# Optimization experiments

Measured on AMD Instinct MI355X. Metric: run time of the kernel, lower is better.

Reference implementation:

```python
import jax, jax.numpy as jnp
import numpy as np

PENALTY = -100.0  # reset penalty used by the torch module


def log_g(x):
    # torch: where(x >= 0, log(relu(x) + 0.5), -softplus(-x))
    return jnp.where(x >= 0, jnp.log(jax.nn.relu(x) + 0.5), -jax.nn.softplus(-x))


def setup_inputs() -> dict:
    key = jax.random.key(0)
    k1, k2, k3 = jax.random.split(key, 3)
    B, S, D = 4, 8192, 1024
    x = jax.random.normal(k1, (B, S, D), dtype=jnp.float32)
    W = jax.random.normal(k2, (D, 2 * D), dtype=jnp.float32) * (1.0 / np.sqrt(D))
    input_ids = jax.random.randint(k3, (B, S), 0, 32000, dtype=jnp.int64)
    return {"x": x, "W": W, "input_ids": input_ids}


def reference(x, W, input_ids):
    # x: [B,S,D], W: [D,2D] (to_hidden_and_gate, no bias), proj_out=False -> Identity
    hg = jnp.einsum("bsd,de->bse", x, W)            # [B,S,2D]
    hidden, gate = jnp.split(hg, 2, axis=-1)          # each [B,S,D]

    pad_mask = input_ids == 0                         # [B,S]

    log_coeffs = -jax.nn.softplus(gate)               # log(1 - z)
    log_z = -jax.nn.softplus(-gate)                   # log z
    log_values = log_z + log_g(hidden)                # log(z * h_tilde)

    # reset at positions following a pad token (shifted mask)
    reset = jnp.pad(pad_mask[:, :-1], ((0, 0), (1, 0)))[:, :, None]  # [B,S,1]

    lc = jnp.where(reset, PENALTY, log_coeffs)
    a_star = jnp.cumsum(lc, axis=1)
    lv = jnp.where(reset, PENALTY, log_values)
    log_h = a_star + jax.lax.cumlogsumexp(lv - a_star, axis=1)
    out = jnp.exp(log_h)                              # [B,S,D]

    next_prev_hidden = jnp.where(pad_mask[:, -1:, None], 0.0, out[:, -1:])
    return out, next_prev_hidden
```

## Files before the change

kernel.cpp:

```cpp
#include <hip/hip_runtime.h>
#include <hip/hip_fp16.h>
#include <math.h>

#define S_LEN 8192
#define D_DIM 1024
#define B_DIM 4
#define M_DIM (B_DIM * S_LEN)
#define BSD   ((size_t)M_DIM * D_DIM)
#define CHN   (B_DIM * D_DIM)
#define CHUNK 64
#define NCH   (S_LEN / CHUNK)

typedef _Float16 f16x8 __attribute__((ext_vector_type(8)));
typedef __attribute__((ext_vector_type(4))) float f32x4;
typedef unsigned int u32;

__device__ __forceinline__ u32 pk2h(float a, float b) {
    auto h = __builtin_amdgcn_cvt_pkrtz(a, b);
    u32 r; __builtin_memcpy(&r, &h, 4); return r;
}

__device__ __forceinline__ void gload16(const void* g, void* l) {
    __builtin_amdgcn_global_load_lds(
        (const __attribute__((address_space(1))) u32*)g,
        (__attribute__((address_space(3))) u32*)l,
        16, 0, 0);
}

__global__ __launch_bounds__(256) void w_to_f16t(
    const float* __restrict__ W, unsigned short* __restrict__ Wt)
{
    __shared__ float T[64][65];
    const int t  = threadIdx.x;
    const int n0 = (int)blockIdx.x * 64;
    const int k0 = (int)blockIdx.y * 64;
    #pragma unroll
    for (int p = 0; p < 4; ++p) {
        int u = p * 256 + t;
        int r = u >> 4, c4 = (u & 15) * 4;
        float4 v = *(const float4*)&W[(size_t)(k0 + r) * 2048 + n0 + c4];
        T[r][c4 + 0] = v.x; T[r][c4 + 1] = v.y;
        T[r][c4 + 2] = v.z; T[r][c4 + 3] = v.w;
    }
    __syncthreads();
    #pragma unroll
    for (int p = 0; p < 2; ++p) {
        int u = p * 256 + t;
        int n = u >> 3, kc = (u & 7) * 8;
        u32 out[4];
        #pragma unroll
        for (int j = 0; j < 4; ++j)
            out[j] = pk2h(T[kc + 2 * j][n], T[kc + 2 * j + 1][n]);
        *(uint4*)&Wt[(size_t)(n0 + n) * 1024 + k0 + kc] = *(uint4*)out;
    }
}

__global__ __launch_bounds__(256) void x_to_f16sw(
    const float* __restrict__ x, unsigned short* __restrict__ xh)
{
    int tid = (int)blockIdx.x * 256 + threadIdx.x;
    int m  = tid >> 7;
    int cg = tid & 127;
    const float4* src = (const float4*)&x[(size_t)m * 1024 + cg * 8];
    float4 v0 = src[0], v1 = src[1];
    u32 o[4] = { pk2h(v0.x, v0.y), pk2h(v0.z, v0.w),
                 pk2h(v1.x, v1.y), pk2h(v1.z, v1.w) };
    int j   = cg & 7;
    int cgd = (cg & ~7) | (j ^ (m & 7));
    *(uint4*)&xh[(size_t)m * 1024 + cgd * 8] = *(uint4*)o;
}

__global__ __launch_bounds__(512, 2) void gemm_8p(
    const unsigned short* __restrict__ xh, const unsigned short* __restrict__ Wt,
    const int* __restrict__ ids, u32* __restrict__ P)
{
    __shared__ __align__(16) unsigned short Ah[2 * 256 * 64];
    __shared__ __align__(16) unsigned short Bt[2 * 256 * 64];

    const int t    = threadIdx.x;
    const int lane = t & 63;
    const int wid  = t >> 6;
    const int wm   = wid >> 2;
    const int wd   = wid & 3;

    const int lin  = (int)blockIdx.x;
    const int xcd  = lin & 7;
    const int slot = lin >> 3;
    const int m0   = (xcd * 16 + (slot >> 3)) * 256;
    const int c0   = (slot & 7) * 128;

    f32x4 accH[8][2], accG[8][2];
    #pragma unroll
    for (int i = 0; i < 8; ++i)
        #pragma unroll
        for (int j = 0; j < 2; ++j) {
            accH[i][j] = (f32x4)0.0f;
            accG[i][j] = (f32x4)0.0f;
        }

    auto stageA = [&](int kb, int buf, int half) {
        char* Ad = (char*)Ah + (buf << 15) + (half << 14);
        #pragma unroll
        for (int i = 0; i < 2; ++i) {
            int sl  = i * 512 + t;
            int row = half * 128 + (sl >> 3);
            int c   = sl & 7;
            const unsigned short* src =
                xh + ((size_t)(m0 + row) << 10) + kb + (c << 3);
            gload16(src, Ad + (size_t)sl * 16);
        }
    };
    auto stageB = [&](int kb, int buf, int half) {
        char* Bd = (char*)Bt + (buf << 15) + (half << 14);
        #pragma unroll
        for (int i = 0; i < 2; ++i) {
            int sl  = i * 512 + t;
            int col = sl >> 3;
            int kc  = (sl & 7) ^ (col & 7);
            const unsigned short* src =
                Wt + ((size_t)(half * 1024 + c0 + col) << 10) + kb + (kc << 3);
            gload16(src, Bd + (size_t)sl * 16);
        }
    };

    auto readA = [&](const char* Ab, int kk, f16x8 a[8]) {
        int chunk = kk * 4 + (lane >> 4);
        #pragma unroll
        for (int mf = 0; mf < 8; ++mf) {
            int row = wm * 128 + mf * 16 + (lane & 15);
            a[mf] = *(const f16x8*)(Ab + row * 128 + ((chunk ^ (row & 7)) << 4));
        }
    };
    auto readB = [&](const char* Bb, int kk, int hg, f16x8 b[2]) {
        int chunk = kk * 4 + (lane >> 4);
        #pragma unroll
        for (int df = 0; df < 2; ++df) {
            int col = wd * 32 + df * 16 + (lane & 15);
            b[df] = *(const f16x8*)(Bb + (hg * 128 + col) * 128
                                       + ((chunk ^ (col & 7)) << 4));
        }
    };

    #define MMA_CLUSTER(ACC, AV, BV)                                       \
        __builtin_amdgcn_s_setprio(1);                                     \
        _Pragma("unroll")                                                  \
        for (int mf = 0; mf < 8; ++mf)                                     \
            _Pragma("unroll")                                              \
            for (int df = 0; df < 2; ++df)                                 \
                ACC[mf][df] = __builtin_amdgcn_mfma_f32_16x16x32_f16(      \
                    AV[mf], BV[df], ACC[mf][df], 0, 0, 0);                 \
        __builtin_amdgcn_s_setprio(0);

    stageA(0, 0, 0); stageA(0, 0, 1); stageB(0, 0, 0); stageB(0, 0, 1);
    asm volatile("s_waitcnt vmcnt(0)" ::: "memory");
    __builtin_amdgcn_sched_barrier(0);
    __builtin_amdgcn_s_barrier();

    for (int tt = 0; tt < 16; ++tt) {
        const int buf   = tt & 1;
        const int kbn   = (tt + 1) << 6;
        const bool more = tt < 15;
        const char* Ab = (const char*)Ah + (buf << 15);
        const char* Bb = (const char*)Bt + (buf << 15);
        f16x8 a0[8], a1[8], bh0[2], bg0[2], bh1[2], bg1[2];

        readA(Ab, 0, a0); readB(Bb, 0, 0, bh0);
        if (more) { stageA(kbn, buf ^ 1, 0); stageA(kbn, buf ^ 1, 1); }
        asm volatile("s_waitcnt lgkmcnt(0)" ::: "memory");
        __builtin_amdgcn_sched_barrier(0);
        readB(Bb, 0, 1, bg0);
        __builtin_amdgcn_sched_barrier(0);
        MMA_CLUSTER(accH, a0, bh0)

        asm volatile("s_waitcnt lgkmcnt(0)" ::: "memory");
        __builtin_amdgcn_sched_barrier(0);
        readA(Ab, 1, a1); readB(Bb, 1, 0, bh1);
        if (more) { stageB(kbn, buf ^ 1, 0); stageB(kbn, buf ^ 1, 1); }
        __builtin_amdgcn_sched_barrier(0);
        MMA_CLUSTER(accG, a0, bg0)

        asm volatile("s_waitcnt lgkmcnt(0)" ::: "memory");
        __builtin_amdgcn_sched_barrier(0);
        readB(Bb, 1, 1, bg1);
        __builtin_amdgcn_sched_barrier(0);
        MMA_CLUSTER(accH, a1, bh1)

        asm volatile("s_waitcnt lgkmcnt(0)" ::: "memory");
        __builtin_amdgcn_sched_barrier(0);
        MMA_CLUSTER(accG, a1, bg1)
        if (more) {
            asm volatile("s_waitcnt vmcnt(0)" ::: "memory");
            __builtin_amdgcn_sched_barrier(0);
            __builtin_amdgcn_s_barrier();
        }
    }
    #undef MMA_CLUSTER

    #pragma unroll
    for (int mf = 0; mf < 8; ++mf) {
        int mbase = m0 + wm * 128 + mf * 16 + (lane >> 4) * 4;
        #pragma unroll
        for (int r = 0; r < 4; ++r) {
            int m = mbase + r;
            int b = m >> 13;
            int s = m & 8191;
            bool reset = (s > 0) && (ids[b * S_LEN + s - 1] == 0);
            #pragma unroll
            for (int df = 0; df < 2; ++df) {
                int d = c0 + wd * 32 + df * 16 + (lane & 15);
                float hid = accH[mf][df][r];
                float g   = accG[mf][df][r];
                float eg  = __expf(-g);
                float z   = 1.0f / (1.0f + eg);
                float c   = eg * z;
                float gt  = (hid >= 0.0f) ? (hid + 0.5f)
                                          : 1.0f / (1.0f + __expf(-hid));
                float v   = z * gt;
                if (reset) { c = 0.0f; v = 0.0f; }
                __half2 h2 = __floats2half2_rn(c, v);
                u32 packed;
                __builtin_memcpy(&packed, &h2, 4);
                P[(size_t)m * D_DIM + d] = packed;
            }
        }
    }
}

__global__ __launch_bounds__(256, 3) void gemm_fb(
    const float* __restrict__ x, const unsigned short* __restrict__ Wt,
    const int* __restrict__ ids, u32* __restrict__ P)
{
    __shared__ __align__(16) unsigned short Ah[128 * 64];
    __shared__ __align__(16) unsigned short Bt[2 * 64 * 64];

    const int t    = threadIdx.x;
    const int lane = t & 63;
    const int wid  = t >> 6;
    const int wm   = wid >> 1;
    const int wd   = wid & 1;

    const int lin  = (int)blockIdx.y * (int)gridDim.x + (int)blockIdx.x;
    const int xcd  = lin & 7;
    const int slot = lin >> 3;
    const int m0   = (xcd * 32 + (slot >> 4)) * 128;
    const int c0   = (slot & 15) * 64;

    f32x4 accH[4][2], accG[4][2];
    #pragma unroll
    for (int i = 0; i < 4; ++i)
        #pragma unroll
        for (int j = 0; j < 2; ++j) {
            accH[i][j] = (f32x4)0.0f;
            accG[i][j] = (f32x4)0.0f;
        }

    for (int kb = 0; kb < 1024; kb += 64) {
        __syncthreads();
        #pragma unroll
        for (int i = 0; i < 4; ++i) {
            int slotb = wid * 256 + i * 64;
            int sl  = slotb + lane;
            int hg  = sl >> 9;
            int col = (sl >> 3) & 63;
            int kc  = (sl & 7) ^ (col & 7);
            const unsigned short* src =
                Wt + ((size_t)(hg * 1024 + c0 + col) << 10) + kb + (kc << 3);
            gload16(src, (char*)Bt + (size_t)slotb * 16);
        }
        #pragma unroll
        for (int p = 0; p < 8; ++p) {
            int s   = p * 256 + t;
            int row = s >> 4;
            int c4  = s & 15;
            float4 v = *(const float4*)&x[(size_t)(m0 + row) * 1024 + kb + c4 * 4];
            uint2 h;
            h.x = pk2h(v.x, v.y);
            h.y = pk2h(v.z, v.w);
            int byte = row * 128 + ((((c4 >> 1) ^ (row & 7))) << 4) + ((c4 & 1) << 3);
            *(uint2*)((char*)Ah + byte) = h;
        }
        __syncthreads();
        #pragma unroll
        for (int kk = 0; kk < 2; ++kk) {
            f16x8 bh[2], bg[2];
            #pragma unroll
            for (int df = 0; df < 2; ++df) {
                int col = wd * 32 + df * 16 + (lane & 15);
                int chunk = kk * 4 + (lane >> 4);
                int byte = col * 128 + ((chunk ^ (col & 7)) << 4);
                bh[df] = *(const f16x8*)((const char*)Bt + byte);
                bg[df] = *(const f16x8*)((const char*)Bt + 8192 + byte);
            }
            #pragma unroll
            for (int mf = 0; mf < 4; ++mf) {
                int row = wm * 64 + mf * 16 + (lane & 15);
                int chunk = kk * 4 + (lane >> 4);
                int byte = row * 128 + ((chunk ^ (row & 7)) << 4);
                f16x8 a = *(const f16x8*)((const char*)Ah + byte);
                #pragma unroll
                for (int df = 0; df < 2; ++df) {
                    accH[mf][df] = __builtin_amdgcn_mfma_f32_16x16x32_f16(
                        a, bh[df], accH[mf][df], 0, 0, 0);
                    accG[mf][df] = __builtin_amdgcn_mfma_f32_16x16x32_f16(
                        a, bg[df], accG[mf][df], 0, 0, 0);
                }
            }
        }
    }

    #pragma unroll
    for (int mf = 0; mf < 4; ++mf) {
        int mbase = m0 + wm * 64 + mf * 16 + (lane >> 4) * 4;
        #pragma unroll
        for (int r = 0; r < 4; ++r) {
            int m = mbase + r;
            int b = m >> 13;
            int s = m & 8191;
            bool reset = (s > 0) && (ids[b * S_LEN + s - 1] == 0);
            #pragma unroll
            for (int df = 0; df < 2; ++df) {
                int d = c0 + wd * 32 + df * 16 + (lane & 15);
                float hid = accH[mf][df][r];
                float g   = accG[mf][df][r];
                float eg  = __expf(-g);
                float z   = 1.0f / (1.0f + eg);
                float c   = eg * z;
                float gt  = (hid >= 0.0f) ? (hid + 0.5f)
                                          : 1.0f / (1.0f + __expf(-hid));
                float v   = z * gt;
                if (reset) { c = 0.0f; v = 0.0f; }
                __half2 h2 = __floats2half2_rn(c, v);
                u32 packed;
                __builtin_memcpy(&packed, &h2, 4);
                P[(size_t)m * D_DIM + d] = packed;
            }
        }
    }
}

__global__ __launch_bounds__(256) void scan_phase_a(
    const u32* __restrict__ P,
    float* __restrict__ Cp, float* __restrict__ Lp)
{
    int ch0 = (blockIdx.x * 256 + threadIdx.x) * 4;
    int c   = blockIdx.y;
    int b   = ch0 >> 10;
    int d0  = ch0 & 1023;
    size_t base = (size_t)b * S_LEN * D_DIM + d0;
    int s0 = c * CHUNK;

    float C[4] = {1.f, 1.f, 1.f, 1.f};
    float H[4] = {0.f, 0.f, 0.f, 0.f};
    for (int s = 0; s < CHUNK; ++s) {
        uint4 q = *(const uint4*)&P[base + (size_t)(s0 + s) * D_DIM];
        u32 qs[4] = {q.x, q.y, q.z, q.w};
        #pragma unroll
        for (int j = 0; j < 4; ++j) {
            __half2 h2;
            __builtin_memcpy(&h2, &qs[j], 4);
            float cc = __low2float(h2);
            float vv = __high2float(h2);
            H[j] = fmaf(cc, H[j], vv);
            C[j] *= cc;
        }
    }
    *(float4*)&Cp[c * CHN + ch0] = *(float4*)C;
    *(float4*)&Lp[c * CHN + ch0] = *(float4*)H;
}

__global__ __launch_bounds__(256) void scan_phase_b(
    const float* __restrict__ Cp, const float* __restrict__ Lp,
    float* __restrict__ carry)
{
    int ch = blockIdx.x * 256 + threadIdx.x;
    float h = 0.0f;
    for (int c = 0; c < NCH; ++c) {
        carry[c * CHN + ch] = h;
        h = fmaf(Cp[c * CHN + ch], h, Lp[c * CHN + ch]);
    }
}

__global__ __launch_bounds__(256) void scan_phase_c(
    u32* __restrict__ Pio,
    const float* __restrict__ carry,
    const int* __restrict__ ids)
{
    int ch0 = (blockIdx.x * 256 + threadIdx.x) * 4;
    int c   = blockIdx.y;
    int b   = ch0 >> 10;
    int d0  = ch0 & 1023;
    size_t base = (size_t)b * S_LEN * D_DIM + d0;
    int s0 = c * CHUNK;

    float H[4];
    *(float4*)H = *(const float4*)&carry[c * CHN + ch0];

    for (int s = 0; s < CHUNK; ++s) {
        size_t idx = base + (size_t)(s0 + s) * D_DIM;
        uint4 q = *(const uint4*)&Pio[idx];
        u32 qs[4] = {q.x, q.y, q.z, q.w};
        u32 os[4];
        #pragma unroll
        for (int j = 0; j < 4; ++j) {
            __half2 h2;
            __builtin_memcpy(&h2, &qs[j], 4);
            float cc = __low2float(h2);
            float vv = __high2float(h2);
            H[j] = fmaf(cc, H[j], vv);
            os[j] = __float_as_uint(H[j]);
        }
        *(uint4*)&Pio[idx] = *(uint4*)os;
    }
    if (c == NCH - 1) {
        bool pad = (ids[b * S_LEN + (S_LEN - 1)] == 0);
        u32 os[4];
        #pragma unroll
        for (int j = 0; j < 4; ++j)
            os[j] = __float_as_uint(pad ? 0.0f : H[j]);
        *(uint4*)&Pio[BSD + (size_t)b * D_DIM + d0] = *(uint4*)os;
    }
}

extern "C" void kernel_launch(void* const* d_in, const int* in_sizes, int n_in,
                              void* d_out, int out_size, void* d_ws, size_t ws_size,
                              hipStream_t stream) {
    const float* x   = (const float*)d_in[0];
    const float* W   = (const float*)d_in[1];
    const int*   ids = (const int*)d_in[2];

    u32* P = (u32*)d_out;
    unsigned short* Wt = (unsigned short*)d_ws;
    float* Cp    = (float*)((char*)d_ws + (size_t) 4 * 1024 * 1024);
    float* Lp    = (float*)((char*)d_ws + (size_t) 6 * 1024 * 1024);
    float* carry = (float*)((char*)d_ws + (size_t) 8 * 1024 * 1024);
    unsigned short* xh = (unsigned short*)((char*)d_ws + (size_t)10 * 1024 * 1024);
    const size_t need = (size_t)10 * 1024 * 1024 + BSD * 2;

    w_to_f16t<<<dim3(32, 16), 256, 0, stream>>>(W, Wt);

    if (ws_size >= need) {
        x_to_f16sw<<<(M_DIM * 128) / 256, 256, 0, stream>>>(x, xh);
        gemm_8p<<<1024, 512, 0, stream>>>(xh, Wt, ids, P);
    } else {
        dim3 ggrid(D_DIM / 64, M_DIM / 128);
        gemm_fb<<<ggrid, 256, 0, stream>>>(x, Wt, ids, P);
    }

    dim3 sgrid(CHN / 1024, NCH);
    scan_phase_a<<<sgrid, 256, 0, stream>>>(P, Cp, Lp);
    scan_phase_b<<<CHN / 256, 256, 0, stream>>>(Cp, Lp, carry);
    scan_phase_c<<<sgrid, 256, 0, stream>>>(P, carry, ids);
}
```

Measured before the change: 272.6 us.

## Load GEMM B operand straight from global into registers with software prefetch

Drops the LDS staging buffer for the weight (B) operand in the fused GEMM. Each wave now loads its B fragments directly from global memory into registers, prefetching the next k-block's fragments between MFMA clusters. The last MFMA cluster of each iteration moves to the start of the next one, and the barrier wait becomes a partial vmcnt. This removes B's LDS writes and reads and halves shared-memory use, but each B element is now fetched from L2 once per wave row instead of once per block. The strided 16-byte global loads also carry more latency that the schedule has to hide.

```diff
diff --git a/kernel.cpp b/kernel.cpp
--- a/kernel.cpp
+++ b/kernel.cpp
@@ -75,7 +75,6 @@
     const int* __restrict__ ids, u32* __restrict__ P)
 {
     __shared__ __align__(16) unsigned short Ah[2 * 256 * 64];
-    __shared__ __align__(16) unsigned short Bt[2 * 256 * 64];
 
     const int t    = threadIdx.x;
     const int lane = t & 63;
@@ -110,18 +109,6 @@
             gload16(src, Ad + (size_t)sl * 16);
         }
     };
-    auto stageB = [&](int kb, int buf, int half) {
-        char* Bd = (char*)Bt + (buf << 15) + (half << 14);
-        #pragma unroll
-        for (int i = 0; i < 2; ++i) {
-            int sl  = i * 512 + t;
-            int col = sl >> 3;
-            int kc  = (sl & 7) ^ (col & 7);
-            const unsigned short* src =
-                Wt + ((size_t)(half * 1024 + c0 + col) << 10) + kb + (kc << 3);
-            gload16(src, Bd + (size_t)sl * 16);
-        }
-    };
 
     auto readA = [&](const char* Ab, int kk, f16x8 a[8]) {
         int chunk = kk * 4 + (lane >> 4);
@@ -131,13 +118,14 @@
             a[mf] = *(const f16x8*)(Ab + row * 128 + ((chunk ^ (row & 7)) << 4));
         }
     };
-    auto readB = [&](const char* Bb, int kk, int hg, f16x8 b[2]) {
+
+    auto loadB = [&](f16x8 b[2], int kb, int kk, int hg) {
         int chunk = kk * 4 + (lane >> 4);
         #pragma unroll
         for (int df = 0; df < 2; ++df) {
             int col = wd * 32 + df * 16 + (lane & 15);
-            b[df] = *(const f16x8*)(Bb + (hg * 128 + col) * 128
-                                       + ((chunk ^ (col & 7)) << 4));
+            b[df] = *(const f16x8*)(Wt + ((size_t)(hg * 1024 + c0 + col) << 10)
+                                       + kb + (chunk << 3));
         }
     };
 
@@ -151,49 +139,43 @@
                     AV[mf], BV[df], ACC[mf][df], 0, 0, 0);                 \
         __builtin_amdgcn_s_setprio(0);
 
-    stageA(0, 0, 0); stageA(0, 0, 1); stageB(0, 0, 0); stageB(0, 0, 1);
+    f16x8 a0[8], a1[8], bh0[2], bg0[2], bh1[2], bg1[2];
+
+    loadB(bh0, 0, 0, 0); loadB(bg0, 0, 0, 1); loadB(bh1, 0, 1, 0);
+    stageA(0, 0, 0); stageA(0, 0, 1);
     asm volatile("s_waitcnt vmcnt(0)" ::: "memory");
     __builtin_amdgcn_sched_barrier(0);
     __builtin_amdgcn_s_barrier();
 
     for (int tt = 0; tt < 16; ++tt) {
         const int buf   = tt & 1;
+        const int kbc   = tt << 6;
         const int kbn   = (tt + 1) << 6;
         const bool more = tt < 15;
         const char* Ab = (const char*)Ah + (buf << 15);
-        const char* Bb = (const char*)Bt + (buf << 15);
-        f16x8 a0[8], a1[8], bh0[2], bg0[2], bh1[2], bg1[2];
-
-        readA(Ab, 0, a0); readB(Bb, 0, 0, bh0);
+
+        if (tt) { MMA_CLUSTER(accG, a1, bg1) }
+        loadB(bg1, kbc, 1, 1);
         if (more) { stageA(kbn, buf ^ 1, 0); stageA(kbn, buf ^ 1, 1); }
+        readA(Ab, 0, a0);
         asm volatile("s_waitcnt lgkmcnt(0)" ::: "memory");
         __builtin_amdgcn_sched_barrier(0);
-        readB(Bb, 0, 1, bg0);
-        __builtin_amdgcn_sched_barrier(0);
         MMA_CLUSTER(accH, a0, bh0)
-
+        if (more) loadB(bh0, kbn, 0, 0);
+        readA(Ab, 1, a1);
+        MMA_CLUSTER(accG, a0, bg0)
+        if (more) loadB(bg0, kbn, 0, 1);
         asm volatile("s_waitcnt lgkmcnt(0)" ::: "memory");
         __builtin_amdgcn_sched_barrier(0);
-        readA(Ab, 1, a1); readB(Bb, 1, 0, bh1);
-        if (more) { stageB(kbn, buf ^ 1, 0); stageB(kbn, buf ^ 1, 1); }
-        __builtin_amdgcn_sched_barrier(0);
-        MMA_CLUSTER(accG, a0, bg0)
-
-        asm volatile("s_waitcnt lgkmcnt(0)" ::: "memory");
-        __builtin_amdgcn_sched_barrier(0);
-        readB(Bb, 1, 1, bg1);
-        __builtin_amdgcn_sched_barrier(0);
         MMA_CLUSTER(accH, a1, bh1)
-
-        asm volatile("s_waitcnt lgkmcnt(0)" ::: "memory");
-        __builtin_amdgcn_sched_barrier(0);
-        MMA_CLUSTER(accG, a1, bg1)
+        if (more) loadB(bh1, kbn, 1, 0);
         if (more) {
-            asm volatile("s_waitcnt vmcnt(0)" ::: "memory");
+            asm volatile("s_waitcnt vmcnt(6)" ::: "memory");
             __builtin_amdgcn_sched_barrier(0);
             __builtin_amdgcn_s_barrier();
         }
     }
+    MMA_CLUSTER(accG, a1, bg1)
     #undef MMA_CLUSTER
 
     #pragma unroll
```

Measured after the change: 304.5 us. 11.7% more time.

## Fuse chunk-level scan aggregate computation into GEMM epilogue

Applied to the files above, without the earlier changes.

The GEMM epilogue now composes each thread's per-row coefficients and values into partial affine (C, L) pairs. It stages them in the reused A shared-memory tile and reduces each 64-row chunk per column, writing the chunk aggregates that scan_phase_a used to produce. This removes the separate scan_phase_a launch and its full re-read of the packed P buffer on the fast path. In exchange the epilogue gains shared-memory traffic, two barriers and extra arithmetic. Aggregates are now computed in fp32 before fp16 rounding rather than from the rounded P values.

```diff
diff --git a/kernel.cpp b/kernel.cpp
--- a/kernel.cpp
+++ b/kernel.cpp
@@ -72,7 +72,8 @@
 
 __global__ __launch_bounds__(512, 2) void gemm_8p(
     const unsigned short* __restrict__ xh, const unsigned short* __restrict__ Wt,
-    const int* __restrict__ ids, u32* __restrict__ P)
+    const int* __restrict__ ids, u32* __restrict__ P,
+    float* __restrict__ Cp, float* __restrict__ Lp)
 {
     __shared__ __align__(16) unsigned short Ah[2 * 256 * 64];
     __shared__ __align__(16) unsigned short Bt[2 * 256 * 64];
@@ -196,9 +197,14 @@
     }
     #undef MMA_CLUSTER
 
+    __builtin_amdgcn_s_barrier();
+    float* Caff = (float*)Ah;
+
     #pragma unroll
     for (int mf = 0; mf < 8; ++mf) {
         int mbase = m0 + wm * 128 + mf * 16 + (lane >> 4) * 4;
+        float Cr[2] = {1.0f, 1.0f};
+        float Lr[2] = {0.0f, 0.0f};
         #pragma unroll
         for (int r = 0; r < 4; ++r) {
             int m = mbase + r;
@@ -221,8 +227,37 @@
                 u32 packed;
                 __builtin_memcpy(&packed, &h2, 4);
                 P[(size_t)m * D_DIM + d] = packed;
+                Lr[df] = fmaf(c, Lr[df], v);
+                Cr[df] *= c;
             }
         }
+        int rq = wm * 32 + mf * 4 + (lane >> 4);
+        #pragma unroll
+        for (int df = 0; df < 2; ++df) {
+            int col = wd * 32 + df * 16 + (lane & 15);
+            Caff[(rq * 128 + col) * 2 + 0] = Cr[df];
+            Caff[(rq * 128 + col) * 2 + 1] = Lr[df];
+        }
+    }
+    __builtin_amdgcn_s_barrier();
+    {
+        int sc  = t >> 7;
+        int col = t & 127;
+        float C = 1.0f, L = 0.0f;
+        #pragma unroll
+        for (int q = 0; q < 16; ++q) {
+            int rq = sc * 16 + q;
+            float cq = Caff[(rq * 128 + col) * 2 + 0];
+            float lq = Caff[(rq * 128 + col) * 2 + 1];
+            L = fmaf(cq, L, lq);
+            C *= cq;
+        }
+        int m    = m0 + sc * 64;
+        int b    = m >> 13;
+        int cidx = (m & 8191) >> 6;
+        int ch   = (b << 10) | (c0 + col);
+        Cp[cidx * CHN + ch] = C;
+        Lp[cidx * CHN + ch] = L;
     }
 }
 
@@ -438,16 +473,16 @@
 
     w_to_f16t<<<dim3(32, 16), 256, 0, stream>>>(W, Wt);
 
+    dim3 sgrid(CHN / 1024, NCH);
     if (ws_size >= need) {
         x_to_f16sw<<<(M_DIM * 128) / 256, 256, 0, stream>>>(x, xh);
-        gemm_8p<<<1024, 512, 0, stream>>>(xh, Wt, ids, P);
+        gemm_8p<<<1024, 512, 0, stream>>>(xh, Wt, ids, P, Cp, Lp);
     } else {
         dim3 ggrid(D_DIM / 64, M_DIM / 128);
         gemm_fb<<<ggrid, 256, 0, stream>>>(x, Wt, ids, P);
-    }
-
-    dim3 sgrid(CHN / 1024, NCH);
-    scan_phase_a<<<sgrid, 256, 0, stream>>>(P, Cp, Lp);
+        scan_phase_a<<<sgrid, 256, 0, stream>>>(P, Cp, Lp);
+    }
+
     scan_phase_b<<<CHN / 256, 256, 0, stream>>>(Cp, Lp, carry);
     scan_phase_c<<<sgrid, 256, 0, stream>>>(P, carry, ids);
 }
```

After: 253.4 us. 1.08x faster.
